# Performance work log

Measured on AMD Instinct MI355X. Metric: run time of the kernel, lower is better.

Reference implementation:

```python
import jax, jax.numpy as jnp
import numpy as np
from jax import lax

OUT_SIZE = 224  # original input spatial size (output_size of anomaly map)
NUM_NEIGHBORS = 9
SIGMA = 4.0
KSIZE = 2 * int(4.0 * SIGMA + 0.5) + 1  # 33, kornia-style kernel size


def avg_pool3(x):
    # AvgPool2d(3, 1, 1), count_include_pad=True -> sum over 3x3 window / 9
    s = lax.reduce_window(x, 0.0, lax.add, (1, 1, 3, 3), (1, 1, 1, 1),
                          [(0, 0), (0, 0), (1, 1), (1, 1)])
    return s / 9.0


def euclidean_dist(x, y):
    # x: [..., N, E], y: [..., M, E] -> [..., N, M]
    x_norm = jnp.sum(x * x, axis=-1, keepdims=True)
    y_norm = jnp.sum(y * y, axis=-1, keepdims=True)
    res = x_norm - 2.0 * jnp.matmul(x, jnp.swapaxes(y, -2, -1)) + jnp.swapaxes(y_norm, -2, -1)
    return jnp.sqrt(jnp.clip(res, 0.0))


def gaussian_blur(x):
    # x: [B,1,H,W]; separable Gaussian, reflect padding (kornia GaussianBlur2d default)
    r = KSIZE // 2
    t = jnp.arange(KSIZE, dtype=x.dtype) - r
    k = jnp.exp(-(t * t) / (2.0 * SIGMA * SIGMA))
    k = k / jnp.sum(k)
    xp = jnp.pad(x, ((0, 0), (0, 0), (r, r), (r, r)), mode='reflect')
    kh = k.reshape(1, 1, KSIZE, 1)
    kw = k.reshape(1, 1, 1, KSIZE)
    y = lax.conv_general_dilated(xp, kh, (1, 1), 'VALID',
                                 dimension_numbers=('NCHW', 'OIHW', 'NCHW'))
    return lax.conv_general_dilated(y, kw, (1, 1), 'VALID',
                                    dimension_numbers=('NCHW', 'OIHW', 'NCHW'))


def compute_anomaly_score(patch_scores, locations, embedding, memory_bank):
    # patch_scores/locations: [B, P]; embedding: [B*P, E]; memory_bank: [M, E]
    batch, num_patches = patch_scores.shape
    bidx = jnp.arange(batch)
    max_patches = jnp.argmax(patch_scores, axis=1)                       # [B]
    max_feats = embedding.reshape(batch, num_patches, -1)[bidx, max_patches]  # [B,E]
    score = patch_scores[bidx, max_patches]                              # [B]
    nn_index = locations[bidx, max_patches]                              # [B]
    nn_sample = memory_bank[nn_index]                                    # [B,E]
    n_nb = min(NUM_NEIGHBORS, memory_bank.shape[0])
    d_bank = euclidean_dist(nn_sample, memory_bank)                      # [B,M]
    _, support = lax.top_k(-d_bank, n_nb)                                # [B,k] smallest
    sup_feats = memory_bank[support]                                     # [B,k,E]
    d = euclidean_dist(max_feats[:, None, :], sup_feats)[:, 0, :]        # [B,k]
    weights = (1.0 - jax.nn.softmax(d, axis=1))[:, 0]                    # [B]
    return weights * score


def setup_inputs() -> dict:
    key = jax.random.key(0)
    k1, k2, k3 = jax.random.split(key, 3)
    feat2 = jax.random.normal(k1, (8, 512, 28, 28), dtype=jnp.float32)
    feat3 = jax.random.normal(k2, (8, 1024, 14, 14), dtype=jnp.float32)
    memory_bank = jax.random.normal(k3, (20000, 1536), dtype=jnp.float32)
    return {'feat2': feat2, 'feat3': feat3, 'memory_bank': memory_bank}


def reference(feat2, feat3, memory_bank):
    # feature pooling (AvgPool2d(3,1,1) on each backbone layer)
    f2 = avg_pool3(feat2)
    f3 = avg_pool3(feat3)
    batch, _, height, width = f2.shape
    # generate_embedding: bilinear upsample deeper layer, concat along channels
    f3u = jax.image.resize(f3, (batch, f3.shape[1], height, width), method='bilinear')
    emb = jnp.concatenate([f2, f3u], axis=1)                 # [B,1536,28,28]
    emb_dim = emb.shape[1]
    embedding = emb.transpose(0, 2, 3, 1).reshape(-1, emb_dim)  # [B*784, 1536]
    # nearest_neighbors with n_neighbors=1
    dist = euclidean_dist(embedding, memory_bank)            # [N, M]
    patch_scores = jnp.min(dist, axis=1)
    locations = jnp.argmin(dist, axis=1)
    patch_scores = patch_scores.reshape(batch, -1)
    locations = locations.reshape(batch, -1)
    pred_score = compute_anomaly_score(patch_scores, locations, embedding, memory_bank)
    # anomaly map: bilinear upsample patch scores to input size + gaussian blur
    score_map = patch_scores.reshape(batch, 1, width, height)
    amap = jax.image.resize(score_map, (batch, 1, OUT_SIZE, OUT_SIZE), method='bilinear')
    anomaly_map = gaussian_blur(amap)
    return anomaly_map, pred_score
```

## Files before the change

### kernel.cpp

```cpp
#include <hip/hip_runtime.h>
#include <math.h>

#define NB 8
#define C2 512
#define C3 1024
#define H2 28
#define W2 28
#define H3 14
#define W3 14
#define EDIM 1536
#define PPB (H2*W2)
#define NPATCH (NB*PPB)
#define MPAD 6400
#define MBANK 20000
#define NBPAD 20096
#define NBG (NBPAD/16)
#define OUTW 224
#define NNB 9
#define KS 33
#define KR 16
#define NMT 25
#define NNTB 157
#define CHUNKS 8
#define CH (MBANK/CHUNKS)
#define MPB 64
#define NSLAB 24
#define GRPB (NSLAB*1024)

#define SXQ 63.5f
#define SYQ (127.0f/6.0f)

typedef __attribute__((ext_vector_type(4))) int   i32x4;

#define LEXLT(va,ia,vb,ib) ((va) < (vb) || ((va)==(vb) && (ia)<(ib)))
#define CSWAP(va,ia,vb,ib) { if (LEXLT(va,ia,vb,ib)) { float _tv=(vb); int _ti=(ib); (vb)=(va); (ib)=(ia); (va)=_tv; (ia)=_ti; } }

#define BAR() asm volatile("s_barrier" ::: "memory")
#define WAITV0() asm volatile("s_waitcnt vmcnt(0)" ::: "memory")

__device__ __forceinline__ void gload16(const void* g, void* l) {
  __builtin_amdgcn_global_load_lds(
      (const __attribute__((address_space(1))) unsigned int*)g,
      (__attribute__((address_space(3))) unsigned int*)l, 16, 0, 0);
}
__device__ __forceinline__ signed char q8(float x, float s) {
  int v = (int)rintf(x * s);
  v = v > 127 ? 127 : (v < -127 ? -127 : v);
  return (signed char)v;
}
__device__ __forceinline__ size_t pk_addr(int row, int c) {
  return ((size_t)((row >> 4)*NSLAB + (c >> 6)) << 10)
       + (((c >> 4) & 3) << 8) + ((row & 15) << 4) + (c & 15);
}


__global__ __launch_bounds__(256) void pool2_kernel(const float* __restrict__ in,
    float* __restrict__ emb32, signed char* __restrict__ embp) {
  int bid = blockIdx.x;
  int cg = bid & 7; int h = (bid >> 3) % H2; int b = bid / (8*H2);
  int t = threadIdx.x;
  __shared__ float s3[3][64][29];
  for (int li = t; li < 3*64*28; li += 256) {
    int w = li % 28; int c = (li/28) & 63; int dh = li/(28*64);
    int hh = h + dh - 1;
    float v = 0.f;
    if (hh >= 0 && hh < H2) v = in[((size_t)(b*C2) + cg*64 + c)*784 + hh*28 + w];
    s3[dh][c][w] = v;
  }
  __syncthreads();
  for (int o = t; o < 64*28; o += 256) {
    int c = o & 63, w = o >> 6;
    float s = 0.f;
    #pragma unroll
    for (int dh = 0; dh < 3; ++dh) {
      s += s3[dh][c][w];
      if (w > 0)  s += s3[dh][c][w-1];
      if (w < 27) s += s3[dh][c][w+1];
    }
    s *= (1.f/9.f);
    int row = b*PPB + h*28 + w;
    int cc = cg*64 + c;
    emb32[(size_t)row*EDIM + cc] = s;
    embp[pk_addr(row, cc)] = q8(s, SXQ);
  }
}

__global__ void pool3_kernel(const float* __restrict__ in, float* __restrict__ f3p) {
  int id = blockIdx.x*blockDim.x + threadIdx.x;
  if (id >= NB*C3*H3*W3) return;
  int w = id % W3, h = (id / W3) % H3, c = (id / (H3*W3)) % C3, b = id / (C3*H3*W3);
  const float* src = in + (size_t)(b*C3 + c)*H3*W3;
  float s = 0.f;
  #pragma unroll
  for (int dh=-1; dh<=1; ++dh) {
    int hh = h+dh; if (hh<0||hh>=H3) continue;
    #pragma unroll
    for (int dw=-1; dw<=1; ++dw) {
      int ww = w+dw; if (ww<0||ww>=W3) continue;
      s += src[hh*W3+ww];
    }
  }
  f3p[(size_t)id] = s * (1.f/9.f);
}

__global__ __launch_bounds__(256) void up3_kernel(const float* __restrict__ f3p,
    float* __restrict__ emb32, signed char* __restrict__ embp) {
  int bid = blockIdx.x;
  int cg = bid & 15; int i = (bid >> 4) % H2; int b = bid / (16*H2);
  int t = threadIdx.x;
  float sy = i*0.5f - 0.25f; sy = fminf(fmaxf(sy,0.f),(float)(H3-1));
  int y0 = (int)sy; int y1 = min(y0+1,H3-1); float fy = sy - (float)y0;
  __shared__ float r2[2][64][15];
  for (int li = t; li < 2*64*14; li += 256) {
    int w = li % 14; int c = (li/14) & 63; int yy = li/(14*64);
    int ysrc = yy ? y1 : y0;
    r2[yy][c][w] = f3p[((size_t)(b*C3) + cg*64 + c)*196 + ysrc*14 + w];
  }
  __syncthreads();
  for (int o = t; o < 64*28; o += 256) {
    int c = o & 63, j = o >> 6;
    float sx = j*0.5f - 0.25f; sx = fminf(fmaxf(sx,0.f),(float)(W3-1));
    int x0 = (int)sx; int x1 = min(x0+1,W3-1); float fx = sx - (float)x0;
    float v = (1.f-fy)*((1.f-fx)*r2[0][c][x0] + fx*r2[0][c][x1])
            +      fy *((1.f-fx)*r2[1][c][x0] + fx*r2[1][c][x1]);
    int row = b*PPB + i*28 + j;
    int cc = C2 + cg*64 + c;
    emb32[(size_t)row*EDIM + cc] = v;
    embp[pk_addr(row, cc)] = q8(v, SXQ);
  }
}


__global__ __launch_bounds__(256) void bank_pack_kernel(const float* __restrict__ bank,
                                                        signed char* __restrict__ bankp,
                                                        float* __restrict__ yn) {
  __shared__ float rn[16];
  int grp = blockIdx.x;
  int t = threadIdx.x;
  if (t < 16) rn[t] = 0.f;
  __syncthreads();
  #pragma unroll
  for (int q = 0; q < 6; ++q) {
    int chunk = t + 256*q;
    int p = chunk >> 6, l = chunk & 63;
    int h = l & 15, gg = l >> 4;
    int row = grp*16 + h;
    int o16[4] = {0,0,0,0};
    if (row < MBANK) {
      const float* src = bank + (size_t)row*EDIM + p*64 + gg*16;
      signed char* oc = (signed char*)o16;
      float ls = 0.f;
      #pragma unroll
      for (int e = 0; e < 16; ++e) { float v = src[e]; ls = fmaf(v, v, ls); oc[e] = q8(v, SYQ); }
      atomicAdd(&rn[h], ls);
    }
    *reinterpret_cast<int4*>(bankp + (size_t)grp*GRPB + (size_t)chunk*16) =
        make_int4(o16[0], o16[1], o16[2], o16[3]);
  }
  __syncthreads();
  if (t < 16 && grp*16 + t < MBANK) yn[grp*16 + t] = rn[t];
}


__global__ __launch_bounds__(512, 4) void dist_min_i8(
    const signed char* __restrict__ Apk, const signed char* __restrict__ Bpk,
    const float* __restrict__ yn, float* __restrict__ outq, int* __restrict__ outi)
{
  __shared__ __align__(16) unsigned char LDSC[32768];
  const int t = threadIdx.x;
  const int lane = t & 63, wid = t >> 6;
  const int wr = wid >> 1, wc = wid & 1;

  const int nwg = NMT*NNTB;
  int orig = blockIdx.x;
  int xcd = orig & 7, loc = orig >> 3;
  int qq = nwg >> 3, rm = nwg & 7;
  int wg = (xcd < rm ? xcd*(qq+1) : rm*(qq+1) + (xcd-rm)*qq) + loc;
  const int mt = wg / NNTB, nt = wg % NNTB;
  const int m0 = mt*256, n0 = nt*128;

  const int gA = (m0 >> 4) + wid*2;
  const signed char* aSrc0 = Apk + (size_t)gA*GRPB + lane*16;
  const signed char* aSrc1 = Apk + (size_t)(gA+1)*GRPB + lane*16;
  const unsigned aDstOff = (unsigned)(wid*2048);

  const signed char* bp[4];
  #pragma unroll
  for (int j = 0; j < 4; ++j) {
    int n16 = (n0 >> 4) + wc*4 + j;
    bp[j] = Bpk + (size_t)n16*GRPB + lane*16;
  }
  const unsigned aRd = (unsigned)((wr*4)*1024 + lane*16);

  i32x4 acc[4][4];
  #pragma unroll
  for (int i = 0; i < 4; ++i)
    #pragma unroll
    for (int j = 0; j < 4; ++j) acc[i][j] = (i32x4){0,0,0,0};

  gload16(aSrc0, (char*)LDSC + aDstOff);
  gload16(aSrc1, (char*)LDSC + aDstOff + 1024);
  WAITV0();
  BAR();

  for (int p = 0; p < NSLAB; ++p) {
    const unsigned sb = (unsigned)(p & 1)*16384u;
    i32x4 bfv[4];
    #pragma unroll
    for (int j = 0; j < 4; ++j)
      bfv[j] = *(const i32x4*)(bp[j] + (size_t)p*1024);
    if (p < NSLAB-1) {
      const unsigned sw = (unsigned)((p+1) & 1)*16384u;
      gload16(aSrc0 + (size_t)(p+1)*1024, (char*)LDSC + sw + aDstOff);
      gload16(aSrc1 + (size_t)(p+1)*1024, (char*)LDSC + sw + aDstOff + 1024);
    }
    i32x4 af[4];
    #pragma unroll
    for (int i = 0; i < 4; ++i)
      af[i] = *(const i32x4*)(LDSC + sb + aRd + i*1024);
    __builtin_amdgcn_s_setprio(1);
    #pragma unroll
    for (int i = 0; i < 4; ++i)
      #pragma unroll
      for (int j = 0; j < 4; ++j)
        acc[i][j] = __builtin_amdgcn_mfma_i32_16x16x64_i8(af[i], bfv[j], acc[i][j], 0, 0, 0);
    __builtin_amdgcn_s_setprio(0);
    WAITV0();
    BAR();
  }

  const float NEG2INV = -2.0f * (2.0f/127.0f) * (6.0f/127.0f);
  const int h = lane & 15, g = lane >> 4;
  float ynv[4];
  #pragma unroll
  for (int j = 0; j < 4; ++j) {
    int col = n0 + wc*64 + j*16 + h;
    ynv[j] = col < MBANK ? yn[col] : INFINITY;
  }
  float* smin = (float*)LDSC;
  int* sidx = (int*)(LDSC + 2048);
  #pragma unroll
  for (int i = 0; i < 4; ++i) {
    #pragma unroll
    for (int r = 0; r < 4; ++r) {
      float v = INFINITY; int ix = 0x7fffffff;
      #pragma unroll
      for (int j = 0; j < 4; ++j) {
        float q = fmaf(NEG2INV, (float)acc[i][j][r], ynv[j]);
        int col = n0 + wc*64 + j*16 + h;
        if (q < v || (q == v && col < ix)) { v = q; ix = col; }
      }
      #pragma unroll
      for (int m = 1; m < 16; m <<= 1) {
        float ov = __shfl_xor(v, m);
        int   oi = __shfl_xor(ix, m);
        if (ov < v || (ov == v && oi < ix)) { v = ov; ix = oi; }
      }
      if (h == 0) {
        int rl = wr*64 + i*16 + g*4 + r;
        smin[rl*2 + wc] = v;
        sidx[rl*2 + wc] = ix;
      }
    }
  }
  __syncthreads();
  if (t < 256) {
    float v0 = smin[t*2], v1 = smin[t*2+1];
    int   i0 = sidx[t*2], i1 = sidx[t*2+1];
    float v; int ix;
    if (LEXLT(v1, i1, v0, i0)) { v = v1; ix = i1; } else { v = v0; ix = i0; }
    int row = m0 + t;
    if (row < NPATCH) {
      outq[(size_t)nt*NPATCH + row] = v;
      outi[(size_t)nt*NPATCH + row] = ix;
    }
  }
}


__global__ __launch_bounds__(256) void minrescore_kernel(
    const float* __restrict__ outq, const int* __restrict__ outi,
    const float* __restrict__ emb32, const float* __restrict__ bank,
    const float* __restrict__ yn, int* __restrict__ loc, float* __restrict__ ps) {
  int w = (blockIdx.x*blockDim.x + threadIdx.x) >> 6;
  int lane = threadIdx.x & 63;
  if (w >= NPATCH) return;
  float bv = INFINITY; int bi = 0x7fffffff;
  for (int s = lane; s < NNTB; s += 64) {
    float v = outq[(size_t)s*NPATCH + w];
    int  ix = outi[(size_t)s*NPATCH + w];
    if (LEXLT(v, ix, bv, bi)) { bv = v; bi = ix; }
  }
  #pragma unroll
  for (int m = 32; m; m >>= 1) {
    float ov = __shfl_xor(bv, m);
    int   oi = __shfl_xor(bi, m);
    if (LEXLT(ov, oi, bv, bi)) { bv = ov; bi = oi; }
  }
  int j = bi;
  if (lane == 0) loc[w] = j;
  const float4* x = reinterpret_cast<const float4*>(emb32 + (size_t)w*EDIM);
  const float4* y = reinterpret_cast<const float4*>(bank + (size_t)j*EDIM);
  float accd = 0.f, accx = 0.f;
  #pragma unroll
  for (int k = 0; k < EDIM/4/64; ++k) {
    float4 a = x[lane + k*64], b = y[lane + k*64];
    accd = fmaf(a.x,b.x,accd); accd = fmaf(a.y,b.y,accd);
    accd = fmaf(a.z,b.z,accd); accd = fmaf(a.w,b.w,accd);
    accx = fmaf(a.x,a.x,accx); accx = fmaf(a.y,a.y,accx);
    accx = fmaf(a.z,a.z,accx); accx = fmaf(a.w,a.w,accx);
  }
  #pragma unroll
  for (int s = 32; s; s >>= 1) { accd += __shfl_xor(accd, s); accx += __shfl_xor(accx, s); }
  if (lane == 0) ps[w] = sqrtf(fmaxf(accx - 2.f*accd + yn[j], 0.f));
}


__global__ void argmax_kernel(const float* __restrict__ ps, const int* __restrict__ loc,
                              float* __restrict__ bscore, int* __restrict__ brow, int* __restrict__ bnn) {
  __shared__ float sv[256]; __shared__ int si[256];
  int b = blockIdx.x, t = threadIdx.x;
  float bv = -INFINITY; int bi = 0x7fffffff;
  for (int p = t; p < PPB; p += 256) {
    float v = ps[b*PPB + p];
    if (v > bv || (v == bv && p < bi)) { bv = v; bi = p; }
  }
  sv[t] = bv; si[t] = bi; __syncthreads();
  for (int s = 128; s; s >>= 1) {
    if (t < s) {
      if (sv[t+s] > sv[t] || (sv[t+s] == sv[t] && si[t+s] < si[t])) { sv[t] = sv[t+s]; si[t] = si[t+s]; }
    }
    __syncthreads();
  }
  if (t == 0) {
    bscore[b] = sv[0];
    brow[b]   = b*PPB + si[0];
    bnn[b]    = loc[b*PPB + si[0]];
  }
}

__global__ __launch_bounds__(256) void dbank_kernel(
    const float* __restrict__ bank, const float* __restrict__ yn,
    const int* __restrict__ bnn, float* __restrict__ dbank)
{
  __shared__ float xs[8][EDIM];
  int t = threadIdx.x;
  for (int idx = t*4; idx < 8*EDIM; idx += 256*4) {
    int b = idx / EDIM, k = idx % EDIM;
    float4 v = *reinterpret_cast<const float4*>(bank + (size_t)bnn[b]*EDIM + k);
    *reinterpret_cast<float4*>(&xs[b][k]) = v;
  }
  __syncthreads();
  int lane = t & 63, w = t >> 6;
  for (int u = 0; u < MPB/4; ++u) {
    int m = blockIdx.x*MPB + u*4 + w;
    if (m < MBANK) {
      const float4* yp = reinterpret_cast<const float4*>(bank + (size_t)m*EDIM);
      float acc[8] = {0.f,0.f,0.f,0.f,0.f,0.f,0.f,0.f};
      for (int k4 = lane; k4 < EDIM/4; k4 += 64) {
        float4 y = yp[k4];
        int k = k4*4;
        #pragma unroll
        for (int b = 0; b < 8; ++b) {
          acc[b] = fmaf(y.x, xs[b][k+0], acc[b]);
          acc[b] = fmaf(y.y, xs[b][k+1], acc[b]);
          acc[b] = fmaf(y.z, xs[b][k+2], acc[b]);
          acc[b] = fmaf(y.w, xs[b][k+3], acc[b]);
        }
      }
      #pragma unroll
      for (int b = 0; b < 8; ++b) {
        float a = acc[b];
        #pragma unroll
        for (int s = 32; s; s >>= 1) a += __shfl_xor(a, s);
        acc[b] = a;
      }
      if (lane == 0) {
        #pragma unroll
        for (int b = 0; b < 8; ++b) {
          int nn = bnn[b];
          float d2 = yn[nn] - 2.f*acc[b] + yn[m];
          dbank[(size_t)b*MBANK + m] = sqrtf(fmaxf(d2, 0.f));
        }
      }
    }
  }
}


__global__ __launch_bounds__(256) void top9_stage1(const float* __restrict__ dbank,
                                                   float* __restrict__ cv, int* __restrict__ ci) {
  int b = blockIdx.x / CHUNKS, ch = blockIdx.x % CHUNKS;
  const float* db = dbank + (size_t)b*MBANK + ch*CH;
  int t = threadIdx.x;

  float v0=INFINITY,v1=INFINITY,v2=INFINITY,v3=INFINITY,v4=INFINITY,
        v5=INFINITY,v6=INFINITY,v7=INFINITY,v8=INFINITY;
  int i0=0x7fffffff,i1=0x7fffffff,i2=0x7fffffff,i3=0x7fffffff,i4=0x7fffffff,
      i5=0x7fffffff,i6=0x7fffffff,i7=0x7fffffff,i8=0x7fffffff;

  for (int s = 0; s < (CH+255)/256; ++s) {
    int m = t + s*256;
    if (m < CH) {
      float nv = db[m]; int ni = ch*CH + m;
      if (LEXLT(nv,ni,v8,i8)) {
        v8 = nv; i8 = ni;
        CSWAP(v8,i8,v7,i7); CSWAP(v7,i7,v6,i6); CSWAP(v6,i6,v5,i5); CSWAP(v5,i5,v4,i4);
        CSWAP(v4,i4,v3,i3); CSWAP(v3,i3,v2,i2); CSWAP(v2,i2,v1,i1); CSWAP(v1,i1,v0,i0);
      }
    }
  }

  __shared__ float sv[256*9];
  __shared__ int   si[256*9];
  __shared__ float rv[256]; __shared__ int ri[256]; __shared__ int rp[256];
  sv[t*9+0]=v0; sv[t*9+1]=v1; sv[t*9+2]=v2; sv[t*9+3]=v3; sv[t*9+4]=v4;
  sv[t*9+5]=v5; sv[t*9+6]=v6; sv[t*9+7]=v7; sv[t*9+8]=v8;
  si[t*9+0]=i0; si[t*9+1]=i1; si[t*9+2]=i2; si[t*9+3]=i3; si[t*9+4]=i4;
  si[t*9+5]=i5; si[t*9+6]=i6; si[t*9+7]=i7; si[t*9+8]=i8;
  __syncthreads();

  for (int r = 0; r < NNB; ++r) {
    float bv = INFINITY; int bix = 0x7fffffff; int bp = -1;
    #pragma unroll
    for (int u = 0; u < 9; ++u) {
      float v = sv[t*9+u]; int ix = si[t*9+u];
      if (LEXLT(v,ix,bv,bix)) { bv = v; bix = ix; bp = t*9+u; }
    }
    rv[t] = bv; ri[t] = bix; rp[t] = bp; __syncthreads();
    for (int s = 128; s; s >>= 1) {
      if (t < s) {
        if (LEXLT(rv[t+s],ri[t+s],rv[t],ri[t])) { rv[t]=rv[t+s]; ri[t]=ri[t+s]; rp[t]=rp[t+s]; }
      }
      __syncthreads();
    }
    if (t == 0) {
      cv[blockIdx.x*NNB + r] = rv[0];
      ci[blockIdx.x*NNB + r] = ri[0];
      sv[rp[0]] = INFINITY; si[rp[0]] = 0x7fffffff;
    }
    __syncthreads();
  }
}


__global__ __launch_bounds__(128) void finalize_kernel(
    const float* __restrict__ cv, const int* __restrict__ ci,
    const float* __restrict__ emb32, const float* __restrict__ bank,
    const float* __restrict__ yn, const int* __restrict__ brow,
    const float* __restrict__ bscore, float* __restrict__ out) {
  __shared__ float sv[128]; __shared__ int si[128];
  __shared__ float wv[128]; __shared__ int wi[128]; __shared__ int wp[128];
  __shared__ int supp[NNB]; __shared__ float ds[NNB];
  int b = blockIdx.x, t = threadIdx.x;
  if (t < CHUNKS*NNB) { sv[t] = cv[b*CHUNKS*NNB + t]; si[t] = ci[b*CHUNKS*NNB + t]; }
  else { sv[t] = INFINITY; si[t] = 0x7fffffff; }
  __syncthreads();
  for (int r = 0; r < NNB; ++r) {
    wv[t] = sv[t]; wi[t] = si[t]; wp[t] = t; __syncthreads();
    for (int s = 64; s; s >>= 1) {
      if (t < s) {
        if (LEXLT(wv[t+s],wi[t+s],wv[t],wi[t])) { wv[t]=wv[t+s]; wi[t]=wi[t+s]; wp[t]=wp[t+s]; }
      }
      __syncthreads();
    }
    if (t == 0) {
      supp[r] = wi[0];
      sv[wp[0]] = INFINITY; si[wp[0]] = 0x7fffffff;
    }
    __syncthreads();
  }
  int lane = t & 63, w = t >> 6;
  int row = brow[b];
  const float* x = emb32 + (size_t)row*EDIM;
  for (int j = w; j < NNB; j += 2) {
    const float* y = bank + (size_t)supp[j]*EDIM;
    float accd = 0.f, accx = 0.f;
    for (int k = lane; k < EDIM; k += 64) {
      float a = x[k];
      accd = fmaf(a, y[k], accd);
      accx = fmaf(a, a, accx);
    }
    #pragma unroll
    for (int s = 32; s; s >>= 1) { accd += __shfl_xor(accd, s); accx += __shfl_xor(accx, s); }
    if (lane == 0) ds[j] = sqrtf(fmaxf(accx - 2.f*accd + yn[supp[j]], 0.f));
  }
  __syncthreads();
  if (t == 0) {
    float mx = -INFINITY;
    #pragma unroll
    for (int j = 0; j < NNB; ++j) mx = fmaxf(mx, ds[j]);
    float s = 0.f;
    #pragma unroll
    for (int j = 0; j < NNB; ++j) s += expf(ds[j] - mx);
    float wgt = 1.f - expf(ds[0] - mx) / s;
    out[b] = wgt * bscore[b];
  }
}


__device__ __forceinline__ int refl224(int x) {
  if (x < 0) return -x;
  if (x > OUTW-1) return 2*(OUTW-1) - x;
  return x;
}

__global__ __launch_bounds__(256) void upblurh_kernel(const float* __restrict__ ps,
                                                      float* __restrict__ tmp) {
  int b = blockIdx.x / OUTW, i = blockIdx.x % OUTW;
  int t = threadIdx.x;
  __shared__ float l[W2];
  __shared__ float graw[KS];
  if (t < KS) {
    float x = (float)t - (float)KR;
    graw[t] = expf(-(x*x) / (2.f*4.f*4.f));
  }
  float sy = ((float)i + 0.5f)*0.125f - 0.5f; sy = fminf(fmaxf(sy,0.f),(float)(H2-1));
  int y0 = (int)sy; int y1 = min(y0+1,H2-1); float fy = sy - (float)y0;
  if (t < W2) {
    const float* p = ps + b*PPB;
    l[t] = (1.f-fy)*p[y0*W2+t] + fy*p[y1*W2+t];
  }
  __syncthreads();
  if (t >= OUTW) return;
  float gsum = 0.f;
  #pragma unroll
  for (int u = 0; u < KS; ++u) gsum += graw[u];
  float winv = 1.f / gsum;
  float s = 0.f;
  #pragma unroll
  for (int v = 0; v < KS; ++v) {
    int jj = refl224(t - KR + v);
    float sx = ((float)jj + 0.5f)*0.125f - 0.5f; sx = fminf(fmaxf(sx,0.f),(float)(W2-1));
    int x0 = (int)sx; int x1 = min(x0+1,W2-1); float fx = sx - (float)x0;
    s = fmaf(graw[v]*winv, (1.f-fx)*l[x0] + fx*l[x1], s);
  }
  tmp[((size_t)b*OUTW + i)*OUTW + t] = s;
}

__global__ __launch_bounds__(256) void blurv_kernel(const float* __restrict__ in,
                                                    float* __restrict__ out) {
  __shared__ float graw[KS];
  int t = threadIdx.x;
  if (t < KS) {
    float x = (float)t - (float)KR;
    graw[t] = expf(-(x*x) / (2.f*4.f*4.f));
  }
  __syncthreads();
  int id = blockIdx.x*blockDim.x + t;
  if (id >= NB*OUTW*OUTW) return;
  float gsum = 0.f;
  #pragma unroll
  for (int u = 0; u < KS; ++u) gsum += graw[u];
  float winv = 1.f / gsum;
  int j = id % OUTW, i = (id/OUTW) % OUTW, b = id/(OUTW*OUTW);
  float s = 0.f;
  #pragma unroll
  for (int u = 0; u < KS; ++u) {
    int ii = refl224(i - KR + u);
    s = fmaf(graw[u]*winv, in[((size_t)b*OUTW + ii)*OUTW + j], s);
  }
  out[id] = s;
}


extern "C" void kernel_launch(void* const* d_in, const int* in_sizes, int n_in,
                              void* d_out, int out_size, void* d_ws, size_t ws_size,
                              hipStream_t stream) {
  const float* feat2 = (const float*)d_in[0];
  const float* feat3 = (const float*)d_in[1];
  const float* bank  = (const float*)d_in[2];
  float* out = (float*)d_out;

  char* base = (char*)d_ws;
  size_t off = 0;
  auto alloc = [&](size_t nbytes) -> char* {
    char* p = base + off;
    off += ((nbytes + 255) & ~(size_t)255);
    return p;
  };
  float*       emb32 = (float*)      alloc((size_t)NPATCH*EDIM*4);
  signed char* embp  = (signed char*)alloc((size_t)(MPAD/16)*GRPB);
  signed char* bankp = (signed char*)alloc((size_t)NBG*GRPB);
  float* f3p    = (float*)alloc((size_t)NB*C3*H3*W3*4);
  float* yn     = (float*)alloc(MBANK*4);
  float* outq   = (float*)alloc((size_t)NNTB*NPATCH*4);
  int*   outi   = (int*)  alloc((size_t)NNTB*NPATCH*4);
  float* ps     = (float*)alloc(NPATCH*4);
  int*   loc    = (int*)  alloc(NPATCH*4);
  float* bscore = (float*)alloc(NB*4);
  int*   brow   = (int*)  alloc(NB*4);
  int*   bnn    = (int*)  alloc(NB*4);
  float* dbank  = (float*)alloc((size_t)NB*MBANK*4);
  float* cv     = (float*)alloc(NB*CHUNKS*NNB*4);
  int*   ci     = (int*)  alloc(NB*CHUNKS*NNB*4);
  float* tmp    = (float*)alloc((size_t)NB*OUTW*OUTW*4);

  pool2_kernel<<<NB*H2*8, 256, 0, stream>>>(feat2, emb32, embp);
  {
    int n = NB*C3*H3*W3;
    pool3_kernel<<<(n+255)/256, 256, 0, stream>>>(feat3, f3p);
  }
  up3_kernel<<<NB*H2*16, 256, 0, stream>>>(f3p, emb32, embp);
  bank_pack_kernel<<<NBG, 256, 0, stream>>>(bank, bankp, yn);

  dist_min_i8<<<NMT*NNTB, 512, 0, stream>>>(embp, bankp, yn, outq, outi);
  minrescore_kernel<<<(NPATCH*64)/256, 256, 0, stream>>>(outq, outi, emb32, bank, yn, loc, ps);

  argmax_kernel<<<NB, 256, 0, stream>>>(ps, loc, bscore, brow, bnn);
  dbank_kernel<<<(MBANK+MPB-1)/MPB, 256, 0, stream>>>(bank, yn, bnn, dbank);
  top9_stage1<<<NB*CHUNKS, 256, 0, stream>>>(dbank, cv, ci);
  finalize_kernel<<<NB, 128, 0, stream>>>(cv, ci, emb32, bank, yn, brow, bscore,
                                          out + NB*OUTW*OUTW);

  {
    upblurh_kernel<<<NB*OUTW, 256, 0, stream>>>(ps, tmp);
    int n = NB*OUTW*OUTW;
    blurv_kernel<<<(n+255)/256, 256, 0, stream>>>(tmp, out);
  }
}
```

Measured before the change: 492.8 us.

## Switch int8 distance GEMM to 32x32x32 MFMA with 32-row packed layout

Repacks both the embedding and memory-bank int8 operands into 32-row by 32-column slabs and replaces the 16x16x64 i8 MFMA with the 32x32x32 i8 variant. Each wave now computes a 2x2 grid of 32x32 tiles instead of a 4x4 grid of 16x16 tiles. The goal is to cut fragment loads per MFMA and use the larger instruction's throughput. The min/argmin epilogue is rewritten for the 32x32 accumulator row mapping, which adds a deeper shuffle reduction and a new index mapping that could be wrong.

```diff
diff --git a/kernel.cpp b/kernel.cpp
--- a/kernel.cpp
+++ b/kernel.cpp
@@ -14,7 +14,8 @@
 #define MPAD 6400
 #define MBANK 20000
 #define NBPAD 20096
-#define NBG (NBPAD/16)
+#define NBG32 (NBPAD/32)
+#define NGA32 (MPAD/32)
 #define OUTW 224
 #define NNB 9
 #define KS 33
@@ -24,13 +25,15 @@
 #define CHUNKS 8
 #define CH (MBANK/CHUNKS)
 #define MPB 64
-#define NSLAB 24
-#define GRPB (NSLAB*1024)
+#define NPH 24
+#define NSLAB32 48
+#define GRPB32 (NSLAB32*1024)
 
 #define SXQ 63.5f
 #define SYQ (127.0f/6.0f)
 
-typedef __attribute__((ext_vector_type(4))) int   i32x4;
+typedef __attribute__((ext_vector_type(4)))  int i32x4;
+typedef __attribute__((ext_vector_type(16))) int i32x16;
 
 #define LEXLT(va,ia,vb,ib) ((va) < (vb) || ((va)==(vb) && (ia)<(ib)))
 #define CSWAP(va,ia,vb,ib) { if (LEXLT(va,ia,vb,ib)) { float _tv=(vb); int _ti=(ib); (vb)=(va); (ib)=(ia); (va)=_tv; (ia)=_ti; } }
@@ -48,9 +51,9 @@
   v = v > 127 ? 127 : (v < -127 ? -127 : v);
   return (signed char)v;
 }
-__device__ __forceinline__ size_t pk_addr(int row, int c) {
-  return ((size_t)((row >> 4)*NSLAB + (c >> 6)) << 10)
-       + (((c >> 4) & 3) << 8) + ((row & 15) << 4) + (c & 15);
+__device__ __forceinline__ size_t pk32_addr(int row, int c) {
+  return ((size_t)((row >> 5)*NSLAB32 + (c >> 5)) << 10)
+       + (((c >> 4) & 1) << 9) + ((row & 31) << 4) + (c & 15);
 }
 
 
@@ -81,7 +84,7 @@
     int row = b*PPB + h*28 + w;
     int cc = cg*64 + c;
     emb32[(size_t)row*EDIM + cc] = s;
-    embp[pk_addr(row, cc)] = q8(s, SXQ);
+    embp[pk32_addr(row, cc)] = q8(s, SXQ);
   }
 }
 
@@ -126,7 +129,7 @@
     int row = b*PPB + i*28 + j;
     int cc = C2 + cg*64 + c;
     emb32[(size_t)row*EDIM + cc] = v;
-    embp[pk_addr(row, cc)] = q8(v, SXQ);
+    embp[pk32_addr(row, cc)] = q8(v, SXQ);
   }
 }
 
@@ -134,31 +137,31 @@
 __global__ __launch_bounds__(256) void bank_pack_kernel(const float* __restrict__ bank,
                                                         signed char* __restrict__ bankp,
                                                         float* __restrict__ yn) {
-  __shared__ float rn[16];
+  __shared__ float rn[32];
   int grp = blockIdx.x;
   int t = threadIdx.x;
-  if (t < 16) rn[t] = 0.f;
-  __syncthreads();
-  #pragma unroll
-  for (int q = 0; q < 6; ++q) {
+  if (t < 32) rn[t] = 0.f;
+  __syncthreads();
+  #pragma unroll
+  for (int q = 0; q < 12; ++q) {
     int chunk = t + 256*q;
-    int p = chunk >> 6, l = chunk & 63;
-    int h = l & 15, gg = l >> 4;
-    int row = grp*16 + h;
+    int s32 = chunk >> 6, l = chunk & 63;
+    int row32 = l & 31, kh = l >> 5;
+    int row = grp*32 + row32;
     int o16[4] = {0,0,0,0};
     if (row < MBANK) {
-      const float* src = bank + (size_t)row*EDIM + p*64 + gg*16;
+      const float* src = bank + (size_t)row*EDIM + s32*32 + kh*16;
       signed char* oc = (signed char*)o16;
       float ls = 0.f;
       #pragma unroll
       for (int e = 0; e < 16; ++e) { float v = src[e]; ls = fmaf(v, v, ls); oc[e] = q8(v, SYQ); }
-      atomicAdd(&rn[h], ls);
-    }
-    *reinterpret_cast<int4*>(bankp + (size_t)grp*GRPB + (size_t)chunk*16) =
+      atomicAdd(&rn[row32], ls);
+    }
+    *reinterpret_cast<int4*>(bankp + (size_t)grp*GRPB32 + (size_t)chunk*16) =
         make_int4(o16[0], o16[1], o16[2], o16[3]);
   }
   __syncthreads();
-  if (t < 16 && grp*16 + t < MBANK) yn[grp*16 + t] = rn[t];
+  if (t < 32 && grp*32 + t < MBANK) yn[grp*32 + t] = rn[t];
 }
 
 
@@ -179,85 +182,88 @@
   const int mt = wg / NNTB, nt = wg % NNTB;
   const int m0 = mt*256, n0 = nt*128;
 
-  const int gA = (m0 >> 4) + wid*2;
-  const signed char* aSrc0 = Apk + (size_t)gA*GRPB + lane*16;
-  const signed char* aSrc1 = Apk + (size_t)(gA+1)*GRPB + lane*16;
-  const unsigned aDstOff = (unsigned)(wid*2048);
-
-  const signed char* bp[4];
-  #pragma unroll
-  for (int j = 0; j < 4; ++j) {
-    int n16 = (n0 >> 4) + wc*4 + j;
-    bp[j] = Bpk + (size_t)n16*GRPB + lane*16;
-  }
-  const unsigned aRd = (unsigned)((wr*4)*1024 + lane*16);
-
-  i32x4 acc[4][4];
-  #pragma unroll
-  for (int i = 0; i < 4; ++i)
-    #pragma unroll
-    for (int j = 0; j < 4; ++j) acc[i][j] = (i32x4){0,0,0,0};
-
-  gload16(aSrc0, (char*)LDSC + aDstOff);
-  gload16(aSrc1, (char*)LDSC + aDstOff + 1024);
+  const signed char* aSrc = Apk + (size_t)((m0 >> 5) + wid)*GRPB32 + lane*16;
+  char* const aDst = (char*)LDSC + wid*2048;
+
+  const signed char* bp[2];
+  #pragma unroll
+  for (int j = 0; j < 2; ++j)
+    bp[j] = Bpk + (size_t)((n0 >> 5) + wc*2 + j)*GRPB32 + lane*16;
+
+  const unsigned aRd = (unsigned)((wr*2)*2048 + lane*16);
+
+  i32x16 acc[2][2];
+  #pragma unroll
+  for (int i = 0; i < 2; ++i)
+    #pragma unroll
+    for (int j = 0; j < 2; ++j)
+      #pragma unroll
+      for (int r = 0; r < 16; ++r) acc[i][j][r] = 0;
+
+  gload16(aSrc,        aDst);
+  gload16(aSrc + 1024, aDst + 1024);
   WAITV0();
   BAR();
 
-  for (int p = 0; p < NSLAB; ++p) {
+  for (int p = 0; p < NPH; ++p) {
     const unsigned sb = (unsigned)(p & 1)*16384u;
-    i32x4 bfv[4];
-    #pragma unroll
-    for (int j = 0; j < 4; ++j)
-      bfv[j] = *(const i32x4*)(bp[j] + (size_t)p*1024);
-    if (p < NSLAB-1) {
+    i32x4 bfv[2][2];
+    #pragma unroll
+    for (int j = 0; j < 2; ++j)
+      #pragma unroll
+      for (int s = 0; s < 2; ++s)
+        bfv[j][s] = *(const i32x4*)(bp[j] + (size_t)(2*p + s)*1024);
+    if (p < NPH-1) {
       const unsigned sw = (unsigned)((p+1) & 1)*16384u;
-      gload16(aSrc0 + (size_t)(p+1)*1024, (char*)LDSC + sw + aDstOff);
-      gload16(aSrc1 + (size_t)(p+1)*1024, (char*)LDSC + sw + aDstOff + 1024);
-    }
-    i32x4 af[4];
-    #pragma unroll
-    for (int i = 0; i < 4; ++i)
-      af[i] = *(const i32x4*)(LDSC + sb + aRd + i*1024);
+      gload16(aSrc + (size_t)(2*(p+1)    )*1024, (char*)LDSC + sw + wid*2048);
+      gload16(aSrc + (size_t)(2*(p+1) + 1)*1024, (char*)LDSC + sw + wid*2048 + 1024);
+    }
+    i32x4 af[2][2];
+    #pragma unroll
+    for (int i = 0; i < 2; ++i)
+      #pragma unroll
+      for (int s = 0; s < 2; ++s)
+        af[i][s] = *(const i32x4*)(LDSC + sb + aRd + i*2048 + s*1024);
     __builtin_amdgcn_s_setprio(1);
     #pragma unroll
-    for (int i = 0; i < 4; ++i)
+    for (int s = 0; s < 2; ++s)
       #pragma unroll
-      for (int j = 0; j < 4; ++j)
-        acc[i][j] = __builtin_amdgcn_mfma_i32_16x16x64_i8(af[i], bfv[j], acc[i][j], 0, 0, 0);
+      for (int i = 0; i < 2; ++i)
+        #pragma unroll
+        for (int j = 0; j < 2; ++j)
+          acc[i][j] = __builtin_amdgcn_mfma_i32_32x32x32_i8(af[i][s], bfv[j][s], acc[i][j], 0, 0, 0);
     __builtin_amdgcn_s_setprio(0);
     WAITV0();
     BAR();
   }
 
   const float NEG2INV = -2.0f * (2.0f/127.0f) * (6.0f/127.0f);
-  const int h = lane & 15, g = lane >> 4;
-  float ynv[4];
-  #pragma unroll
-  for (int j = 0; j < 4; ++j) {
-    int col = n0 + wc*64 + j*16 + h;
-    ynv[j] = col < MBANK ? yn[col] : INFINITY;
+  const int l31 = lane & 31, hi5 = lane >> 5;
+  float ynv[2]; int colv[2];
+  #pragma unroll
+  for (int j = 0; j < 2; ++j) {
+    colv[j] = n0 + wc*64 + j*32 + l31;
+    ynv[j] = colv[j] < MBANK ? yn[colv[j]] : INFINITY;
   }
   float* smin = (float*)LDSC;
   int* sidx = (int*)(LDSC + 2048);
   #pragma unroll
-  for (int i = 0; i < 4; ++i) {
-    #pragma unroll
-    for (int r = 0; r < 4; ++r) {
-      float v = INFINITY; int ix = 0x7fffffff;
+  for (int i = 0; i < 2; ++i) {
+    #pragma unroll
+    for (int r = 0; r < 16; ++r) {
+      float q0 = fmaf(NEG2INV, (float)acc[i][0][r], ynv[0]);
+      float q1 = fmaf(NEG2INV, (float)acc[i][1][r], ynv[1]);
+      float v; int ix;
+      if (LEXLT(q1, colv[1], q0, colv[0])) { v = q1; ix = colv[1]; }
+      else { v = q0; ix = colv[0]; }
       #pragma unroll
-      for (int j = 0; j < 4; ++j) {
-        float q = fmaf(NEG2INV, (float)acc[i][j][r], ynv[j]);
-        int col = n0 + wc*64 + j*16 + h;
-        if (q < v || (q == v && col < ix)) { v = q; ix = col; }
-      }
-      #pragma unroll
-      for (int m = 1; m < 16; m <<= 1) {
+      for (int m = 1; m < 32; m <<= 1) {
         float ov = __shfl_xor(v, m);
         int   oi = __shfl_xor(ix, m);
         if (ov < v || (ov == v && oi < ix)) { v = ov; ix = oi; }
       }
-      if (h == 0) {
-        int rl = wr*64 + i*16 + g*4 + r;
+      if (l31 == 0) {
+        int rl = wr*64 + i*32 + (r&3) + 8*(r>>2) + 4*hi5;
         smin[rl*2 + wc] = v;
         sidx[rl*2 + wc] = ix;
       }
@@ -580,8 +586,8 @@
     return p;
   };
   float*       emb32 = (float*)      alloc((size_t)NPATCH*EDIM*4);
-  signed char* embp  = (signed char*)alloc((size_t)(MPAD/16)*GRPB);
-  signed char* bankp = (signed char*)alloc((size_t)NBG*GRPB);
+  signed char* embp  = (signed char*)alloc((size_t)NGA32*GRPB32);
+  signed char* bankp = (signed char*)alloc((size_t)NBG32*GRPB32);
   float* f3p    = (float*)alloc((size_t)NB*C3*H3*W3*4);
   float* yn     = (float*)alloc(MBANK*4);
   float* outq   = (float*)alloc((size_t)NNTB*NPATCH*4);
@@ -602,7 +608,7 @@
     pool3_kernel<<<(n+255)/256, 256, 0, stream>>>(feat3, f3p);
   }
   up3_kernel<<<NB*H2*16, 256, 0, stream>>>(f3p, emb32, embp);
-  bank_pack_kernel<<<NBG, 256, 0, stream>>>(bank, bankp, yn);
+  bank_pack_kernel<<<NBG32, 256, 0, stream>>>(bank, bankp, yn);
 
   dist_min_i8<<<NMT*NNTB, 512, 0, stream>>>(embp, bankp, yn, outq, outi);
   minrescore_kernel<<<(NPATCH*64)/256, 256, 0, stream>>>(outq, outi, emb32, bank, yn, loc, ps);
```

Result: slower. 549.3 us (+11.5%).

## Deepen int8 distance GEMM pipeline with triple-buffered LDS and register-prefetched B

Applied to the files above, without the earlier changes.

The A-slab staging in the int8 distance/min kernel goes from double to triple buffering in LDS, with loads issued two slabs ahead. B fragments are now double-buffered in registers and fetched one slab ahead. The per-iteration wait is relaxed from vmcnt(0) to vmcnt(6), so global loads overlap with the MFMA work. In exchange, LDS per block grows from 32 KB to 48 KB, which can lower the number of resident blocks per CU, and register pressure rises.

```diff
diff --git a/kernel.cpp b/kernel.cpp
--- a/kernel.cpp
+++ b/kernel.cpp
@@ -36,6 +36,7 @@
 #define CSWAP(va,ia,vb,ib) { if (LEXLT(va,ia,vb,ib)) { float _tv=(vb); int _ti=(ib); (vb)=(va); (ib)=(ia); (va)=_tv; (ia)=_ti; } }
 
 #define BAR() asm volatile("s_barrier" ::: "memory")
+#define WAITV6() asm volatile("s_waitcnt vmcnt(6)" ::: "memory")
 #define WAITV0() asm volatile("s_waitcnt vmcnt(0)" ::: "memory")
 
 __device__ __forceinline__ void gload16(const void* g, void* l) {
@@ -166,7 +167,7 @@
     const signed char* __restrict__ Apk, const signed char* __restrict__ Bpk,
     const float* __restrict__ yn, float* __restrict__ outq, int* __restrict__ outi)
 {
-  __shared__ __align__(16) unsigned char LDSC[32768];
+  __shared__ __align__(16) unsigned char LDSC[49152];
   const int t = threadIdx.x;
   const int lane = t & 63, wid = t >> 6;
   const int wr = wid >> 1, wc = wid & 1;
@@ -198,34 +199,55 @@
     #pragma unroll
     for (int j = 0; j < 4; ++j) acc[i][j] = (i32x4){0,0,0,0};
 
+  i32x4 bfv0[4], bfv1[4];
+
   gload16(aSrc0, (char*)LDSC + aDstOff);
   gload16(aSrc1, (char*)LDSC + aDstOff + 1024);
-  WAITV0();
+  gload16(aSrc0 + 1024, (char*)LDSC + 16384u + aDstOff);
+  gload16(aSrc1 + 1024, (char*)LDSC + 16384u + aDstOff + 1024);
+  #pragma unroll
+  for (int j = 0; j < 4; ++j) bfv0[j] = *(const i32x4*)(bp[j]);
+  WAITV6();
   BAR();
 
+  #pragma unroll 2
   for (int p = 0; p < NSLAB; ++p) {
-    const unsigned sb = (unsigned)(p & 1)*16384u;
-    i32x4 bfv[4];
-    #pragma unroll
-    for (int j = 0; j < 4; ++j)
-      bfv[j] = *(const i32x4*)(bp[j] + (size_t)p*1024);
+    const unsigned sb = (unsigned)(p % 3) * 16384u;
+    const bool even = (p & 1) == 0;
     if (p < NSLAB-1) {
-      const unsigned sw = (unsigned)((p+1) & 1)*16384u;
-      gload16(aSrc0 + (size_t)(p+1)*1024, (char*)LDSC + sw + aDstOff);
-      gload16(aSrc1 + (size_t)(p+1)*1024, (char*)LDSC + sw + aDstOff + 1024);
+      if (even) {
+        #pragma unroll
+        for (int j = 0; j < 4; ++j) bfv1[j] = *(const i32x4*)(bp[j] + (size_t)(p+1)*1024);
+      } else {
+        #pragma unroll
+        for (int j = 0; j < 4; ++j) bfv0[j] = *(const i32x4*)(bp[j] + (size_t)(p+1)*1024);
+      }
+    }
+    if (p < NSLAB-2) {
+      const unsigned sw = (unsigned)((p+2) % 3) * 16384u;
+      gload16(aSrc0 + (size_t)(p+2)*1024, (char*)LDSC + sw + aDstOff);
+      gload16(aSrc1 + (size_t)(p+2)*1024, (char*)LDSC + sw + aDstOff + 1024);
     }
     i32x4 af[4];
     #pragma unroll
     for (int i = 0; i < 4; ++i)
       af[i] = *(const i32x4*)(LDSC + sb + aRd + i*1024);
     __builtin_amdgcn_s_setprio(1);
-    #pragma unroll
-    for (int i = 0; i < 4; ++i)
+    if (even) {
       #pragma unroll
-      for (int j = 0; j < 4; ++j)
-        acc[i][j] = __builtin_amdgcn_mfma_i32_16x16x64_i8(af[i], bfv[j], acc[i][j], 0, 0, 0);
+      for (int i = 0; i < 4; ++i)
+        #pragma unroll
+        for (int j = 0; j < 4; ++j)
+          acc[i][j] = __builtin_amdgcn_mfma_i32_16x16x64_i8(af[i], bfv0[j], acc[i][j], 0, 0, 0);
+    } else {
+      #pragma unroll
+      for (int i = 0; i < 4; ++i)
+        #pragma unroll
+        for (int j = 0; j < 4; ++j)
+          acc[i][j] = __builtin_amdgcn_mfma_i32_16x16x64_i8(af[i], bfv1[j], acc[i][j], 0, 0, 0);
+    }
     __builtin_amdgcn_s_setprio(0);
-    WAITV0();
+    if (p < NSLAB-2) { WAITV6(); } else { WAITV0(); }
     BAR();
   }
 
```

Result: no change. 485.5 us, median of 2 (-1.5%).
